# Kernel tuning notes

Measured on AMD Instinct MI355X. Metric: run time of the kernel, lower is better.

## Reference

```python
import jax, jax.numpy as jnp
import numpy as np

EPS = 1e-06


def setup_inputs() -> dict:
    key = jax.random.key(0)
    ks = jax.random.split(key, 6)
    B, H, S, W = 1, 12, 768, 32
    attn_logits = jax.random.normal(ks[0], (B, H, S, S), dtype=jnp.float32)
    # shared first linear: Linear(1, mlp_width) -> weight [W,1], bias [W]
    W_in = jax.random.normal(ks[1], (W, 1), dtype=jnp.float32) * (1.0)
    b_in = jax.random.normal(ks[2], (W,), dtype=jnp.float32) * 0.1
    # per-head output linear: Linear(mlp_width, 1) -> weight [H, W], bias [H]
    W_out = jax.random.normal(ks[3], (H, W), dtype=jnp.float32) / np.sqrt(W)
    b_out = jax.random.normal(ks[4], (H,), dtype=jnp.float32) * 0.1
    c = jnp.asarray(0.1, dtype=jnp.float32)
    L_multiplier = jnp.asarray(1.0, dtype=jnp.float32)
    init_L = jnp.asarray(512.0, dtype=jnp.float32)  # requires_grad=False in torch
    return {"attn_logits": attn_logits, "W_in": W_in, "b_in": b_in,
            "W_out": W_out, "b_out": b_out, "c": c,
            "L_multiplier": L_multiplier, "init_L": init_L}


def reference(attn_logits, W_in, b_in, W_out, b_out, c, L_multiplier, init_L):
    # gates and reverse cumulative sum along the key axis
    gates = jax.nn.sigmoid(attn_logits)                      # [B,H,S,S]
    pos = jax.lax.cumsum(gates, axis=3, reverse=True)        # flip-cumsum-flip
    numerator = jnp.log(jnp.abs(c * pos) + 1.0)
    max_pos = pos[..., 0:1]                                  # [B,H,S,1]
    threshold = jnp.abs(L_multiplier * init_L)
    denominator = jnp.log(jnp.abs(c * jnp.minimum(max_pos, threshold)) + 1.0) + EPS
    dist = numerator / denominator                           # [B,H,S,S]
    # shared Linear(1,W) + ReLU, then per-head Linear(W,1)
    w1 = W_in[:, 0]                                          # [W]
    hidden = jax.nn.relu(dist[..., None] * w1 + b_in)        # [B,H,S,S,W]
    fire_bias = jnp.einsum('bhijw,hw->bhij', hidden, W_out) + b_out[None, :, None, None]
    return fire_bias
```

## Files before the change

kernel.cpp:

```cpp
#include <hip/hip_runtime.h>
#include <math.h>

#define EPS_F 1e-6f
#define S_DIM 768
#define W_DIM 32
#define H_DIM 12
#define NK 33


__global__ __launch_bounds__(512) void cope_setup_kernel(
    const float* __restrict__ W_in, const float* __restrict__ b_in,
    const float* __restrict__ W_out, const float* __restrict__ b_out,
    float* __restrict__ ws)
{
    __shared__ float th[W_DIM];
    __shared__ int   rk[W_DIM];
    const int t = threadIdx.x;

    if (t < W_DIM) {
        float w1 = W_in[t], b = b_in[t];
        th[t] = (w1 != 0.0f) ? (-b / w1) : __builtin_inff();
    }
    __syncthreads();

    if (t < W_DIM) {
        float mine = th[t];
        int r = 0;
        for (int v = 0; v < W_DIM; v++) {
            float o = th[v];
            if (o < mine || (o == mine && v < t)) r++;
        }
        rk[t] = r;
        ws[r] = mine;
    }
    __syncthreads();

    if (t < H_DIM * NK) {
        int h = t / NK, k = t % NK;
        float A = 0.0f, B = b_out[h];
        for (int w = 0; w < W_DIM; w++) {
            float w1 = W_in[w], bv = b_in[w], ov = W_out[h * W_DIM + w];
            bool active = (w1 > 0.0f) ? (k > rk[w])
                        : (w1 < 0.0f) ? (k <= rk[w])
                        : (bv > 0.0f);
            if (active) { A += w1 * ov; B += bv * ov; }
        }
        ws[W_DIM + h * 2 * NK + 2 * k]     = A;
        ws[W_DIM + h * 2 * NK + 2 * k + 1] = B;
    }
}

__global__ __launch_bounds__(256) void cope_fire_kernel(
    const float* __restrict__ attn,
    const float* __restrict__ c_p,
    const float* __restrict__ Lm_p,
    const float* __restrict__ iL_p,
    const float* __restrict__ ws,
    float* __restrict__ out)
{
    const int t    = threadIdx.x;
    const int lane = t & 63;
    const int wave = t >> 6;
    const int row  = blockIdx.x * 4 + wave;
    const int h    = blockIdx.x / (S_DIM / 4);

    __shared__ __align__(16) float sh[W_DIM];
    __shared__ __align__(8)  float sAB[2 * NK];

    if (t < W_DIM)  sh[t]  = ws[t];
    if (t < 2 * NK) sAB[t] = ws[W_DIM + h * 2 * NK + t];

    const float s3 = ws[3],  s7 = ws[7],  s11 = ws[11], s15 = ws[15];
    const float s19 = ws[19], s23 = ws[23], s27 = ws[27];
    const float c   = c_p[0];
    const float thr = fabsf(Lm_p[0] * iL_p[0]);

    const float* rowp = attn + (size_t)row * S_DIM + lane * 12;
    float4 v0 = *(const float4*)(rowp);
    float4 v1 = *(const float4*)(rowp + 4);
    float4 v2 = *(const float4*)(rowp + 8);
    float g[12] = { v0.x, v0.y, v0.z, v0.w, v1.x, v1.y, v1.z, v1.w,
                    v2.x, v2.y, v2.z, v2.w };
#pragma unroll
    for (int i = 0; i < 12; i++)
        g[i] = __builtin_amdgcn_rcpf(1.0f + __expf(-g[i]));

    float T0 = 0.0f;
#pragma unroll
    for (int i = 0; i < 12; i++) T0 += g[i];
    float P = T0;
#pragma unroll
    for (int d = 1; d < 64; d <<= 1) {
        float y = __shfl_up(P, d, 64);
        if (lane >= d) P += y;
    }
    const float total = __shfl(P, 63, 64);
    const float base  = total - P + T0;

    const float den      = __logf(fabsf(c * fminf(total, thr)) + 1.0f) + EPS_F;
    const float inv_den2 = 0.69314718056f * __builtin_amdgcn_rcpf(den);

    __syncthreads();

    float dv[12];
    {
        float e = 0.0f;
#pragma unroll
        for (int i = 0; i < 12; i++) {
            float pos = base - e;
            e += g[i];
            dv[i] = __log2f(fabsf(c * pos) + 1.0f) * inv_den2;
        }
    }

    float o[12];
#pragma unroll
    for (int half = 0; half < 2; half++) {
        const int i0 = half * 6;

        int    k4[6];
        float4 r[6];
#pragma unroll
        for (int j = 0; j < 6; j++) {
            const float d = dv[i0 + j];
            int k = 0;
            bool b1 = (s15 < d);             if (b1) k += 16;
            float l2 = b1 ? s23 : s7;
            bool b2 = (l2 < d);              if (b2) k += 8;
            float l3a = b2 ? s11 : s3;
            float l3b = b2 ? s27 : s19;
            float l3  = b1 ? l3b : l3a;
            if (l3 < d) k += 4;
            k4[j] = k;
        }
#pragma unroll
        for (int j = 0; j < 6; j++)
            r[j] = *(const float4*)(&sh[k4[j]]);

        float2 ab[6];
        float  dd[6];
#pragma unroll
        for (int j = 0; j < 6; j++) {
            const float d = dv[i0 + j];
            int k = k4[j];
            bool c2 = (r[j].y < d);          if (c2) k += 2;
            float f1 = c2 ? r[j].z : r[j].x;
            bool c1 = (f1 < d);              if (c1) k += 1;
            float f0 = c1 ? (c2 ? r[j].w : r[j].y) : f1;
            if (f0 < d) k += 1;
            ab[j] = *(const float2*)(&sAB[2 * k]);
            dd[j] = d;
        }
#pragma unroll
        for (int j = 0; j < 6; j++)
            o[i0 + j] = fmaf(dd[j], ab[j].x, ab[j].y);
    }

    float* op = out + (size_t)row * S_DIM + lane * 12;
    *(float4*)(op)     = make_float4(o[0], o[1], o[2],  o[3]);
    *(float4*)(op + 4) = make_float4(o[4], o[5], o[6],  o[7]);
    *(float4*)(op + 8) = make_float4(o[8], o[9], o[10], o[11]);
}

extern "C" void kernel_launch(void* const* d_in, const int* in_sizes, int n_in,
                              void* d_out, int out_size, void* d_ws, size_t ws_size,
                              hipStream_t stream) {
    const float* attn  = (const float*)d_in[0];
    const float* W_in  = (const float*)d_in[1];
    const float* b_in  = (const float*)d_in[2];
    const float* W_out = (const float*)d_in[3];
    const float* b_out = (const float*)d_in[4];
    const float* c_p   = (const float*)d_in[5];
    const float* Lm_p  = (const float*)d_in[6];
    const float* iL_p  = (const float*)d_in[7];
    float* out = (float*)d_out;
    float* ws  = (float*)d_ws;

    cope_setup_kernel<<<1, 512, 0, stream>>>(W_in, b_in, W_out, b_out, ws);

    const int rows = H_DIM * S_DIM;
    cope_fire_kernel<<<rows / 4, 256, 0, stream>>>(
        attn, c_p, Lm_p, iL_p, ws, out);
}
```

Before: 104.1 us.

## Fuse weight-setup kernel into main kernel, recomputing tables per block

Removes the single-block setup kernel and its workspace round-trip. Each block now computes the sorted ReLU thresholds and the per-head piecewise-linear A/B coefficients in shared memory, splitting the W reduction across 4 threads per segment. The global attention loads are issued before this setup work so their latency overlaps with it. This saves a kernel launch and the serial dependency between the two kernels, at the cost of redundant setup work and extra barriers in every block.

```diff
diff --git a/kernel.cpp b/kernel.cpp
--- a/kernel.cpp
+++ b/kernel.cpp
@@ -8,54 +8,13 @@
 #define NK 33
 
 
-__global__ __launch_bounds__(512) void cope_setup_kernel(
+__global__ __launch_bounds__(256) void cope_fused_kernel(
+    const float* __restrict__ attn,
     const float* __restrict__ W_in, const float* __restrict__ b_in,
     const float* __restrict__ W_out, const float* __restrict__ b_out,
-    float* __restrict__ ws)
-{
-    __shared__ float th[W_DIM];
-    __shared__ int   rk[W_DIM];
-    const int t = threadIdx.x;
-
-    if (t < W_DIM) {
-        float w1 = W_in[t], b = b_in[t];
-        th[t] = (w1 != 0.0f) ? (-b / w1) : __builtin_inff();
-    }
-    __syncthreads();
-
-    if (t < W_DIM) {
-        float mine = th[t];
-        int r = 0;
-        for (int v = 0; v < W_DIM; v++) {
-            float o = th[v];
-            if (o < mine || (o == mine && v < t)) r++;
-        }
-        rk[t] = r;
-        ws[r] = mine;
-    }
-    __syncthreads();
-
-    if (t < H_DIM * NK) {
-        int h = t / NK, k = t % NK;
-        float A = 0.0f, B = b_out[h];
-        for (int w = 0; w < W_DIM; w++) {
-            float w1 = W_in[w], bv = b_in[w], ov = W_out[h * W_DIM + w];
-            bool active = (w1 > 0.0f) ? (k > rk[w])
-                        : (w1 < 0.0f) ? (k <= rk[w])
-                        : (bv > 0.0f);
-            if (active) { A += w1 * ov; B += bv * ov; }
-        }
-        ws[W_DIM + h * 2 * NK + 2 * k]     = A;
-        ws[W_DIM + h * 2 * NK + 2 * k + 1] = B;
-    }
-}
-
-__global__ __launch_bounds__(256) void cope_fire_kernel(
-    const float* __restrict__ attn,
     const float* __restrict__ c_p,
     const float* __restrict__ Lm_p,
     const float* __restrict__ iL_p,
-    const float* __restrict__ ws,
     float* __restrict__ out)
 {
     const int t    = threadIdx.x;
@@ -66,19 +25,64 @@
 
     __shared__ __align__(16) float sh[W_DIM];
     __shared__ __align__(8)  float sAB[2 * NK];
-
-    if (t < W_DIM)  sh[t]  = ws[t];
-    if (t < 2 * NK) sAB[t] = ws[W_DIM + h * 2 * NK + t];
-
-    const float s3 = ws[3],  s7 = ws[7],  s11 = ws[11], s15 = ws[15];
-    const float s19 = ws[19], s23 = ws[23], s27 = ws[27];
-    const float c   = c_p[0];
-    const float thr = fabsf(Lm_p[0] * iL_p[0]);
+    __shared__ float th_s[W_DIM];
+    __shared__ float sWin[W_DIM], sBin[W_DIM], sWout[W_DIM];
+    __shared__ int   rk_s[W_DIM];
+    __shared__ float pA[4 * NK], pB[4 * NK];
 
     const float* rowp = attn + (size_t)row * S_DIM + lane * 12;
     float4 v0 = *(const float4*)(rowp);
     float4 v1 = *(const float4*)(rowp + 4);
     float4 v2 = *(const float4*)(rowp + 8);
+    const float c   = c_p[0];
+    const float thr = fabsf(Lm_p[0] * iL_p[0]);
+
+    if (t < W_DIM) {
+        float w1 = W_in[t], b = b_in[t];
+        th_s[t] = (w1 != 0.0f) ? (-b / w1) : __builtin_inff();
+        sWin[t] = w1;
+        sBin[t] = b;
+        sWout[t] = W_out[h * W_DIM + t];
+    }
+    __syncthreads();
+
+    if (t < W_DIM) {
+        float mine = th_s[t];
+        int r = 0;
+        for (int v = 0; v < W_DIM; v++) {
+            float o = th_s[v];
+            if (o < mine || (o == mine && v < t)) r++;
+        }
+        rk_s[t] = r;
+        sh[r]   = mine;
+    }
+    __syncthreads();
+
+    if (t < 4 * NK) {
+        const int k = t >> 2, q = t & 3;
+        float A = 0.0f, B = 0.0f;
+#pragma unroll
+        for (int j = 0; j < 8; j++) {
+            const int w = q * 8 + j;
+            float w1 = sWin[w], bv = sBin[w], ov = sWout[w];
+            int   r  = rk_s[w];
+            bool active = (w1 > 0.0f) ? (k > r)
+                        : (w1 < 0.0f) ? (k <= r)
+                        : (bv > 0.0f);
+            if (active) { A += w1 * ov; B += bv * ov; }
+        }
+        pA[t] = A;
+        pB[t] = B;
+    }
+    __syncthreads();
+
+    if (t < NK) {
+        float A = (pA[4*t] + pA[4*t+1]) + (pA[4*t+2] + pA[4*t+3]);
+        float B = (pB[4*t] + pB[4*t+1]) + (pB[4*t+2] + pB[4*t+3]) + b_out[h];
+        sAB[2*t]     = A;
+        sAB[2*t + 1] = B;
+    }
+
     float g[12] = { v0.x, v0.y, v0.z, v0.w, v1.x, v1.y, v1.z, v1.w,
                     v2.x, v2.y, v2.z, v2.w };
 #pragma unroll
@@ -100,8 +104,6 @@
     const float den      = __logf(fabsf(c * fminf(total, thr)) + 1.0f) + EPS_F;
     const float inv_den2 = 0.69314718056f * __builtin_amdgcn_rcpf(den);
 
-    __syncthreads();
-
     float dv[12];
     {
         float e = 0.0f;
@@ -112,6 +114,11 @@
             dv[i] = __log2f(fabsf(c * pos) + 1.0f) * inv_den2;
         }
     }
+
+    __syncthreads();
+
+    const float s3  = sh[3],  s7  = sh[7],  s11 = sh[11], s15 = sh[15];
+    const float s19 = sh[19], s23 = sh[23], s27 = sh[27];
 
     float o[12];
 #pragma unroll
@@ -174,11 +181,9 @@
     const float* Lm_p  = (const float*)d_in[6];
     const float* iL_p  = (const float*)d_in[7];
     float* out = (float*)d_out;
-    float* ws  = (float*)d_ws;
-
-    cope_setup_kernel<<<1, 512, 0, stream>>>(W_in, b_in, W_out, b_out, ws);
+    (void)d_ws; (void)ws_size;
 
     const int rows = H_DIM * S_DIM;
-    cope_fire_kernel<<<rows / 4, 256, 0, stream>>>(
-        attn, c_p, Lm_p, iL_p, ws, out);
+    cope_fused_kernel<<<rows / 4, 256, 0, stream>>>(
+        attn, W_in, b_in, W_out, b_out, c_p, Lm_p, iL_p, out);
 }
```

Result: no change. 103.7 us (-0.4%).
